# Kernel tuning notes

Hardware: AMD Instinct MI355X
Metric: run time of the kernel (lower is better)

Reference implementation:

```python
import jax, jax.numpy as jnp
import numpy as np

B, S, D, H = 2, 2048, 1024, 16
HD = D // H  # head_dim = 64

def setup_inputs() -> dict:
    key = jax.random.key(0)
    ks = jax.random.split(key, 10)
    s = 1.0 / np.sqrt(D)
    return {
        "hidden_states": jax.random.normal(ks[0], (B, S, D), jnp.float32),
        "attention_mask": jnp.ones((B, S), jnp.float32),
        "q_w": jax.random.uniform(ks[1], (D, D), jnp.float32, -s, s),
        "q_b": jax.random.uniform(ks[2], (D,), jnp.float32, -s, s),
        "k_w": jax.random.uniform(ks[3], (D, D), jnp.float32, -s, s),
        "k_b": jax.random.uniform(ks[4], (D,), jnp.float32, -s, s),
        "v_w": jax.random.uniform(ks[5], (D, D), jnp.float32, -s, s),
        "v_b": jax.random.uniform(ks[6], (D,), jnp.float32, -s, s),
        "o_w": jax.random.uniform(ks[7], (D, D), jnp.float32, -s, s),
        "o_b": jax.random.uniform(ks[8], (D,), jnp.float32, -s, s),
    }

def reference(hidden_states, attention_mask, q_w, q_b, k_w, k_b, v_w, v_b, o_w, o_b):
    scale = HD ** -0.5
    # projections; torch Linear: x @ W^T + b. Here weights stored as (D, D) used directly.
    q = hidden_states @ q_w + q_b  # [B,S,D]
    k = hidden_states @ k_w + k_b
    v = hidden_states @ v_w + v_b
    # split heads -> [B,H,S,HD]
    q = q.reshape(B, S, H, HD).transpose(0, 2, 1, 3)
    k = k.reshape(B, S, H, HD).transpose(0, 2, 1, 3)
    v = v.reshape(B, S, H, HD).transpose(0, 2, 1, 3)
    scores = jnp.einsum('bhqd,bhkd->bhqk', q, k) * scale  # [B,H,S,S]
    # additive mask from 2D [B,S] mask (1=keep, 0=mask)
    scores = scores + (1.0 - attention_mask)[:, None, None, :] * -10000.0
    attn = jax.nn.softmax(scores, axis=-1)
    ctx = jnp.einsum('bhqk,bhkd->bhqd', attn, v)  # [B,H,S,HD]
    ctx = ctx.transpose(0, 2, 1, 3).reshape(B, S, D)
    return ctx @ o_w + o_b
```

## Files before the change

### kernel.cpp

```cpp
#include <hip/hip_runtime.h>
#include <hip/hip_bf16.h>

#define B_ 2
#define S_ 2048
#define D_ 1024
#define H_ 16
#define HD_ 64

#define QSCALE 0.18033688f
#define MLOG2E 14426.950408f

typedef __attribute__((ext_vector_type(8))) short bf16x8;
typedef __attribute__((ext_vector_type(4))) short short4v;
typedef __attribute__((ext_vector_type(4))) float floatx4;

static __device__ __forceinline__ float bf2f(short u) {
  union { float f; unsigned int i; } c;
  c.i = ((unsigned int)(unsigned short)u) << 16;
  return c.f;
}
static __device__ __forceinline__ short f2bf(float f) {
  union { float f; unsigned int i; } c; c.f = f;
  unsigned int r = c.i + 0x7FFFu + ((c.i >> 16) & 1u);
  return (short)(r >> 16);
}
static __device__ __forceinline__ short f2bf_fast(float f) {
  union { float f; unsigned int i; } c; c.f = f;
  return (short)((c.i + 0x8000u) >> 16);
}

static __device__ __forceinline__ void gld_lds16(const void* g, void* l) {
  __builtin_amdgcn_global_load_lds(
      (const __attribute__((address_space(1))) unsigned int*)g,
      (__attribute__((address_space(3))) unsigned int*)l, 16, 0, 0);
}

__global__ __launch_bounds__(256)
void prep(const float* __restrict__ w0, const float* __restrict__ w1,
          const float* __restrict__ w2, const float* __restrict__ w3,
          const float* __restrict__ hs, short* __restrict__ WT,
          short* __restrict__ Xb) {
  const int z = blockIdx.z;
  if (z < 4) {
    __shared__ short t[64][65];
    const float* src = z == 0 ? w0 : z == 1 ? w1 : z == 2 ? w2 : w3;
    short* dst = WT + (size_t)z * D_ * D_;
    const int tx = threadIdx.x & 63, ty = threadIdx.x >> 6;
    const int r0 = blockIdx.y * 64, c0 = blockIdx.x * 64;
    for (int r = ty; r < 64; r += 4)
      t[r][tx] = f2bf(src[(size_t)(r0 + r) * D_ + c0 + tx]);
    __syncthreads();
    for (int r = ty; r < 64; r += 4)
      dst[(size_t)(c0 + r) * D_ + r0 + tx] = t[tx][r];
  } else {
    const int bid = blockIdx.y * 16 + blockIdx.x;
    const float4* in4 = (const float4*)hs;
    short4v* out4 = (short4v*)Xb;
#pragma unroll
    for (int i = 0; i < 16; i++) {
      const int idx = bid * 4096 + i * 256 + threadIdx.x;
      const float4 v = in4[idx];
      short4v o;
      o[0] = f2bf(v.x); o[1] = f2bf(v.y); o[2] = f2bf(v.z); o[3] = f2bf(v.w);
      out4[idx] = o;
    }
  }
}

__global__ __launch_bounds__(256, 3)
void gemm_qkv(const short* __restrict__ X, const short* __restrict__ WT,
              const float* __restrict__ qb, const float* __restrict__ kb,
              const float* __restrict__ vb, const float* __restrict__ mask,
              short* __restrict__ Qo, short* __restrict__ Ko,
              short* __restrict__ Vt) {
  __shared__ __align__(16) short As[128 * 32];
  __shared__ __align__(16) short Bs[128 * 32];
  const int tid = threadIdx.x;
  const int wave = tid >> 6, lane = tid & 63;
  const int col = lane & 15, quad = lane >> 4;
  const int m0 = blockIdx.x * 128;
  const int nt = blockIdx.y;
  const int widx = nt >> 3;
  const int n1 = (nt & 7) * 128;
  const short* Bsrc = WT + (size_t)widx * D_ * D_ + (size_t)n1 * D_;
  const int b = m0 >> 11;

  const int srow = tid >> 2;
  const int skcol = (tid & 3) * 8;
  const short* ga = X + (size_t)(m0 + srow) * D_ + skcol;
  const short* gb = Bsrc + (size_t)srow * D_ + skcol;
  short* la = As + tid * 8;
  short* lb = Bs + tid * 8;

  floatx4 acc[4][4];
#pragma unroll
  for (int i = 0; i < 4; i++)
#pragma unroll
    for (int j = 0; j < 4; j++) acc[i][j] = floatx4{0.f, 0.f, 0.f, 0.f};

  if (widx < 2) {
    const int wseq = (wave >> 1) * 64;
    const int wfeat = (wave & 1) * 64;
    for (int k0 = 0; k0 < D_; k0 += 32) {
      gld_lds16(ga, la);
      gld_lds16(ga + 64 * D_, la + 2048);
      gld_lds16(gb, lb);
      gld_lds16(gb + 64 * D_, lb + 2048);
      ga += 32; gb += 32;
      __syncthreads();
      bf16x8 xf[4], wf[4];
#pragma unroll
      for (int j = 0; j < 4; j++)
        xf[j] = *(const bf16x8*)(As + (wseq + j * 16 + col) * 32 + quad * 8);
#pragma unroll
      for (int i = 0; i < 4; i++)
        wf[i] = *(const bf16x8*)(Bs + (wfeat + i * 16 + col) * 32 + quad * 8);
#pragma unroll
      for (int i = 0; i < 4; i++)
#pragma unroll
        for (int j = 0; j < 4; j++)
          acc[i][j] = __builtin_amdgcn_mfma_f32_16x16x32_bf16(wf[i], xf[j],
                                                              acc[i][j], 0, 0, 0);
      __syncthreads();
    }
    const float* bias = widx == 0 ? qb : kb;
    short* dst = widx == 0 ? Qo : Ko;
    const float scale = widx == 0 ? QSCALE : 1.0f;
#pragma unroll
    for (int i = 0; i < 4; i++) {
      const int nf = n1 + wfeat + i * 16 + quad * 4;
      const int h = nf >> 6, hd = nf & 63;
      const float4 bv = *(const float4*)(bias + nf);
#pragma unroll
      for (int j = 0; j < 4; j++) {
        const int s = (m0 + wseq + j * 16 + col) & (S_ - 1);
        short4v pk;
        pk[0] = f2bf((acc[i][j][0] + bv.x) * scale);
        pk[1] = f2bf((acc[i][j][1] + bv.y) * scale);
        pk[2] = f2bf((acc[i][j][2] + bv.z) * scale);
        pk[3] = f2bf((acc[i][j][3] + bv.w) * scale);
        *(short4v*)(dst + ((size_t)(b * H_ + h) * S_ + s) * HD_ + hd) = pk;
      }
    }
  } else {
    const int wrow = (wave & 1) * 64;
    const int wcol = (wave >> 1) * 64;
    for (int k0 = 0; k0 < D_; k0 += 32) {
      gld_lds16(ga, la);
      gld_lds16(ga + 64 * D_, la + 2048);
      gld_lds16(gb, lb);
      gld_lds16(gb + 64 * D_, lb + 2048);
      ga += 32; gb += 32;
      __syncthreads();
      bf16x8 af[4], bfr[4];
#pragma unroll
      for (int i = 0; i < 4; i++)
        af[i] = *(const bf16x8*)(As + (wrow + i * 16 + col) * 32 + quad * 8);
#pragma unroll
      for (int j = 0; j < 4; j++)
        bfr[j] = *(const bf16x8*)(Bs + (wcol + j * 16 + col) * 32 + quad * 8);
#pragma unroll
      for (int i = 0; i < 4; i++)
#pragma unroll
        for (int j = 0; j < 4; j++)
          acc[i][j] = __builtin_amdgcn_mfma_f32_16x16x32_bf16(af[i], bfr[j],
                                                              acc[i][j], 0, 0, 0);
      __syncthreads();
    }
    float bv[4];
#pragma unroll
    for (int j = 0; j < 4; j++) bv[j] = vb[n1 + wcol + j * 16 + col];
    const float* mkb = mask + (size_t)b * S_;
#pragma unroll
    for (int i = 0; i < 4; i++) {
      const int s = (m0 + wrow + i * 16 + quad * 4) & (S_ - 1);
      const float4 mv = *(const float4*)(mkb + s);
      float w[4];
      w[0] = exp2f((mv.x - 1.0f) * MLOG2E);
      w[1] = exp2f((mv.y - 1.0f) * MLOG2E);
      w[2] = exp2f((mv.z - 1.0f) * MLOG2E);
      w[3] = exp2f((mv.w - 1.0f) * MLOG2E);
#pragma unroll
      for (int j = 0; j < 4; j++) {
        const int nl = n1 + wcol + j * 16 + col;
        const int h = nl >> 6, hd = nl & 63;
        short4v pk;
#pragma unroll
        for (int r = 0; r < 4; r++) pk[r] = f2bf((acc[i][j][r] + bv[j]) * w[r]);
        *(short4v*)(Vt + ((size_t)(b * H_ + h) * HD_ + hd) * S_ + s) = pk;
      }
    }
  }
}

__global__ __launch_bounds__(256, 2)
void attn(const short* __restrict__ Q, const short* __restrict__ K,
          const short* __restrict__ Vt, const float* __restrict__ mask,
          short* __restrict__ ctx) {
  __shared__ __align__(16) short Ks[2][4096];
  __shared__ __align__(16) short Vs[2][4096];
  __shared__ __align__(16) short P[4][2][16][72];
  __shared__ __align__(16) short Ws[S_];
  const int tid = threadIdx.x, wave = tid >> 6, lane = tid & 63;
  const int col = lane & 15, quad = lane >> 4;
  const int lin = blockIdx.x;
  const int qt = (lin >> 3) & 15;
  const int gi = (lin & 7) + ((lin >> 7) << 3);
  const int h = gi & 15, b = gi >> 4;
  const short* Qh = Q + (size_t)(b * H_ + h) * S_ * HD_;
  const short* Kh = K + (size_t)(b * H_ + h) * S_ * HD_;
  const short* Vh = Vt + (size_t)(b * H_ + h) * HD_ * S_;
  const float* mk = mask + (size_t)b * S_;
  const int q0 = qt * 128 + wave * 32;

  const int r1 = tid >> 3, c1 = (tid & 7) ^ (r1 & 7);
  const int r2 = r1 + 32,  c2 = (tid & 7) ^ (r2 & 7);
  const int swz = quad ^ (col & 7);

  gld_lds16(Kh + (size_t)r1 * HD_ + c1 * 8, &Ks[0][tid * 8]);
  gld_lds16(Kh + (size_t)r2 * HD_ + c2 * 8, &Ks[0][(tid + 256) * 8]);
  gld_lds16(Vh + (size_t)r1 * S_ + c1 * 8, &Vs[0][tid * 8]);
  gld_lds16(Vh + (size_t)r2 * S_ + c2 * 8, &Vs[0][(tid + 256) * 8]);

  for (int i = tid; i < S_; i += 256)
    Ws[i] = f2bf(exp2f((mk[i] - 1.0f) * MLOG2E));

  bf16x8 qf[2][2];
#pragma unroll
  for (int g = 0; g < 2; g++) {
    const short* qp = Qh + (size_t)(q0 + g * 16 + col) * HD_;
    qf[g][0] = *(const bf16x8*)(qp + quad * 8);
    qf[g][1] = *(const bf16x8*)(qp + 32 + quad * 8);
  }

  floatx4 acc[2][4], rsacc[2];
#pragma unroll
  for (int g = 0; g < 2; g++) {
    rsacc[g] = floatx4{0.f, 0.f, 0.f, 0.f};
#pragma unroll
    for (int d = 0; d < 4; d++) acc[g][d] = floatx4{0.f, 0.f, 0.f, 0.f};
  }

  __syncthreads();

  for (int it = 0; it < S_ / 64; it++) {
    const int buf = it & 1;
    const int kt = it * 64;
    if (it + 1 < S_ / 64) {
      const int kn = kt + 64;
      gld_lds16(Kh + (size_t)(kn + r1) * HD_ + c1 * 8, &Ks[buf ^ 1][tid * 8]);
      gld_lds16(Kh + (size_t)(kn + r2) * HD_ + c2 * 8, &Ks[buf ^ 1][(tid + 256) * 8]);
      gld_lds16(Vh + (size_t)r1 * S_ + kn + c1 * 8, &Vs[buf ^ 1][tid * 8]);
      gld_lds16(Vh + (size_t)r2 * S_ + kn + c2 * 8, &Vs[buf ^ 1][(tid + 256) * 8]);
    }

    bf16x8 kf[4][2];
#pragma unroll
    for (int t = 0; t < 4; t++) {
      const short* kp = &Ks[buf][(t * 16 + col) * 64];
      kf[t][0] = *(const bf16x8*)(kp + swz * 8);
      kf[t][1] = *(const bf16x8*)(kp + (swz ^ 4) * 8);
    }

#pragma unroll
    for (int g = 0; g < 2; g++)
#pragma unroll
      for (int t = 0; t < 4; t++) {
        floatx4 z = floatx4{0.f, 0.f, 0.f, 0.f};
        z = __builtin_amdgcn_mfma_f32_16x16x32_bf16(kf[t][0], qf[g][0], z, 0, 0, 0);
        z = __builtin_amdgcn_mfma_f32_16x16x32_bf16(kf[t][1], qf[g][1], z, 0, 0, 0);
        short4v pk;
#pragma unroll
        for (int r = 0; r < 4; r++) pk[r] = f2bf_fast(exp2f(z[r]));
        *(short4v*)&P[wave][g][col][t * 16 + quad * 4] = pk;
      }

    bf16x8 pf[2][2];
#pragma unroll
    for (int g = 0; g < 2; g++)
#pragma unroll
      for (int kk = 0; kk < 2; kk++)
        pf[g][kk] = *(const bf16x8*)&P[wave][g][col][kk * 32 + quad * 8];

    bf16x8 wf[2];
#pragma unroll
    for (int kk = 0; kk < 2; kk++)
      wf[kk] = *(const bf16x8*)&Ws[kt + kk * 32 + quad * 8];

#pragma unroll
    for (int g = 0; g < 2; g++) {
      rsacc[g] = __builtin_amdgcn_mfma_f32_16x16x32_bf16(wf[0], pf[g][0], rsacc[g], 0, 0, 0);
      rsacc[g] = __builtin_amdgcn_mfma_f32_16x16x32_bf16(wf[1], pf[g][1], rsacc[g], 0, 0, 0);
    }
#pragma unroll
    for (int d = 0; d < 4; d++) {
      const short* vp = &Vs[buf][(d * 16 + col) * 64];
      const bf16x8 vf0 = *(const bf16x8*)(vp + swz * 8);
      const bf16x8 vf1 = *(const bf16x8*)(vp + (swz ^ 4) * 8);
#pragma unroll
      for (int g = 0; g < 2; g++) {
        acc[g][d] = __builtin_amdgcn_mfma_f32_16x16x32_bf16(vf0, pf[g][0], acc[g][d], 0, 0, 0);
        acc[g][d] = __builtin_amdgcn_mfma_f32_16x16x32_bf16(vf1, pf[g][1], acc[g][d], 0, 0, 0);
      }
    }
    __syncthreads();
  }

#pragma unroll
  for (int g = 0; g < 2; g++) {
    const float inv = 1.0f / (rsacc[g][0] + 1e-30f);
    const size_t row = (size_t)b * S_ + q0 + g * 16 + col;
#pragma unroll
    for (int d = 0; d < 4; d++) {
      short4v o;
#pragma unroll
      for (int r = 0; r < 4; r++) o[r] = f2bf(acc[g][d][r] * inv);
      *(short4v*)(ctx + row * D_ + h * HD_ + d * 16 + quad * 4) = o;
    }
  }
}

__global__ __launch_bounds__(256, 2)
void gemm_out(const short* __restrict__ X, const short* __restrict__ WT,
              const float* __restrict__ ob, float* __restrict__ out) {
  __shared__ __align__(16) short As[64 * 32];
  __shared__ __align__(16) short Bs[128 * 32];
  const int tid = threadIdx.x;
  const int wave = tid >> 6, lane = tid & 63;
  const int col = lane & 15, quad = lane >> 4;
  const int m0 = blockIdx.x * 64;
  const int n0 = blockIdx.y * 128;
  const short* Bsrc = WT + (size_t)n0 * D_;
  const int wrow = (wave & 1) * 32;
  const int wcol = (wave >> 1) * 64;

  floatx4 acc[2][4];
#pragma unroll
  for (int i = 0; i < 2; i++)
#pragma unroll
    for (int j = 0; j < 4; j++) acc[i][j] = floatx4{0.f, 0.f, 0.f, 0.f};

  const int arow = tid >> 2, akcol = (tid & 3) * 8;
  const short* ga = X + (size_t)(m0 + arow) * D_ + akcol;
  const short* gb = Bsrc + (size_t)arow * D_ + akcol;
  short* la = As + tid * 8;
  short* lb = Bs + tid * 8;

  for (int k0 = 0; k0 < D_; k0 += 32) {
    gld_lds16(ga, la);
    gld_lds16(gb, lb);
    gld_lds16(gb + 64 * D_, lb + 2048);
    ga += 32; gb += 32;
    __syncthreads();
    bf16x8 af[2], bfr[4];
#pragma unroll
    for (int i = 0; i < 2; i++)
      af[i] = *(const bf16x8*)(As + (wrow + i * 16 + col) * 32 + quad * 8);
#pragma unroll
    for (int j = 0; j < 4; j++)
      bfr[j] = *(const bf16x8*)(Bs + (wcol + j * 16 + col) * 32 + quad * 8);
#pragma unroll
    for (int i = 0; i < 2; i++)
#pragma unroll
      for (int j = 0; j < 4; j++)
        acc[i][j] = __builtin_amdgcn_mfma_f32_16x16x32_bf16(af[i], bfr[j],
                                                            acc[i][j], 0, 0, 0);
    __syncthreads();
  }

  float bv[4];
#pragma unroll
  for (int j = 0; j < 4; j++) bv[j] = ob[n0 + wcol + j * 16 + col];

#pragma unroll
  for (int i = 0; i < 2; i++) {
    const int m = m0 + wrow + i * 16 + quad * 4;
#pragma unroll
    for (int j = 0; j < 4; j++) {
      const int n = n0 + wcol + j * 16 + col;
#pragma unroll
      for (int r = 0; r < 4; r++)
        out[(size_t)(m + r) * D_ + n] = acc[i][j][r] + bv[j];
    }
  }
}

extern "C" void kernel_launch(void* const* d_in, const int* in_sizes, int n_in,
                              void* d_out, int out_size, void* d_ws, size_t ws_size,
                              hipStream_t stream) {
  (void)in_sizes; (void)n_in; (void)out_size; (void)ws_size;
  const float* hs  = (const float*)d_in[0];
  const float* msk = (const float*)d_in[1];
  const float* qw  = (const float*)d_in[2];
  const float* qb  = (const float*)d_in[3];
  const float* kw  = (const float*)d_in[4];
  const float* kb  = (const float*)d_in[5];
  const float* vw  = (const float*)d_in[6];
  const float* vb  = (const float*)d_in[7];
  const float* ow  = (const float*)d_in[8];
  const float* ob  = (const float*)d_in[9];
  float* out = (float*)d_out;
  char* ws = (char*)d_ws;

  short* Xb  = (short*)(ws);
  short* WT  = (short*)(ws + (8ull  << 20));
  short* Qp  = (short*)(ws + (16ull << 20));
  short* Kp  = (short*)(ws + (24ull << 20));
  short* Vtp = (short*)(ws + (32ull << 20));
  short* Ctx = Xb;

  prep<<<dim3(16, 16, 5), 256, 0, stream>>>(qw, kw, vw, ow, hs, WT, Xb);
  gemm_qkv<<<dim3(32, 24), 256, 0, stream>>>(Xb, WT, qb, kb, vb, msk, Qp, Kp, Vtp);
  attn<<<dim3(512), 256, 0, stream>>>(Qp, Kp, Vtp, msk, Ctx);
  gemm_out<<<dim3(64, 8), 256, 0, stream>>>(Ctx, WT + 3ull * D_ * D_, ob, out);
}
```

Baseline: 212.6 us.

## Double attention query tile per block to 256 rows, halving grid

Each wave now handles 64 query rows instead of 32, so each block covers 256 queries. The grid shrinks from 512 to 256 blocks, which halves redundant K/V tile loads per head and amortizes each LDS K/V fragment over more MFMAs. The P scratch buffer is reused in ping-pong fashion across query groups, with a narrower row pitch and 8-byte reads. The cost is higher register pressure (launch bounds dropped to 1 block/SM) and only 256 blocks, which may underfill the GPU's compute units.

```diff
diff --git a/kernel.cpp b/kernel.cpp
--- a/kernel.cpp
+++ b/kernel.cpp
@@ -193,25 +193,25 @@
   }
 }
 
-__global__ __launch_bounds__(256, 2)
+__global__ __launch_bounds__(256, 1)
 void attn(const short* __restrict__ Q, const short* __restrict__ K,
           const short* __restrict__ Vt, const float* __restrict__ mask,
           short* __restrict__ ctx) {
   __shared__ __align__(16) short Ks[2][4096];
   __shared__ __align__(16) short Vs[2][4096];
-  __shared__ __align__(16) short P[4][2][16][72];
+  __shared__ __align__(16) short P[4][2][16][68];
   __shared__ __align__(16) short Ws[S_];
   const int tid = threadIdx.x, wave = tid >> 6, lane = tid & 63;
   const int col = lane & 15, quad = lane >> 4;
   const int lin = blockIdx.x;
-  const int qt = (lin >> 3) & 15;
-  const int gi = (lin & 7) + ((lin >> 7) << 3);
-  const int h = gi & 15, b = gi >> 4;
-  const short* Qh = Q + (size_t)(b * H_ + h) * S_ * HD_;
-  const short* Kh = K + (size_t)(b * H_ + h) * S_ * HD_;
-  const short* Vh = Vt + (size_t)(b * H_ + h) * HD_ * S_;
+  const int qt = (lin >> 3) & 7;
+  const int bh = (lin & 7) | ((lin >> 6) << 3);
+  const int h = bh & 15, b = bh >> 4;
+  const short* Qh = Q + (size_t)bh * S_ * HD_;
+  const short* Kh = K + (size_t)bh * S_ * HD_;
+  const short* Vh = Vt + (size_t)bh * HD_ * S_;
   const float* mk = mask + (size_t)b * S_;
-  const int q0 = qt * 128 + wave * 32;
+  const int q0 = qt * 256 + wave * 64;
 
   const int r1 = tid >> 3, c1 = (tid & 7) ^ (r1 & 7);
   const int r2 = r1 + 32,  c2 = (tid & 7) ^ (r2 & 7);
@@ -225,17 +225,17 @@
   for (int i = tid; i < S_; i += 256)
     Ws[i] = f2bf(exp2f((mk[i] - 1.0f) * MLOG2E));
 
-  bf16x8 qf[2][2];
-#pragma unroll
-  for (int g = 0; g < 2; g++) {
+  bf16x8 qf[4][2];
+#pragma unroll
+  for (int g = 0; g < 4; g++) {
     const short* qp = Qh + (size_t)(q0 + g * 16 + col) * HD_;
     qf[g][0] = *(const bf16x8*)(qp + quad * 8);
     qf[g][1] = *(const bf16x8*)(qp + 32 + quad * 8);
   }
 
-  floatx4 acc[2][4], rsacc[2];
-#pragma unroll
-  for (int g = 0; g < 2; g++) {
+  floatx4 acc[4][4], rsacc[4];
+#pragma unroll
+  for (int g = 0; g < 4; g++) {
     rsacc[g] = floatx4{0.f, 0.f, 0.f, 0.f};
 #pragma unroll
     for (int d = 0; d < 4; d++) acc[g][d] = floatx4{0.f, 0.f, 0.f, 0.f};
@@ -262,8 +262,12 @@
       kf[t][1] = *(const bf16x8*)(kp + (swz ^ 4) * 8);
     }
 
-#pragma unroll
-    for (int g = 0; g < 2; g++)
+    bf16x8 pf[4][2];
+    bf16x8 wf0 = *(const bf16x8*)&Ws[kt + quad * 8];
+    bf16x8 wf1 = *(const bf16x8*)&Ws[kt + 32 + quad * 8];
+#pragma unroll
+    for (int g = 0; g < 4; g++) {
+      const int pb = g & 1;
 #pragma unroll
       for (int t = 0; t < 4; t++) {
         floatx4 z = floatx4{0.f, 0.f, 0.f, 0.f};
@@ -272,33 +276,28 @@
         short4v pk;
 #pragma unroll
         for (int r = 0; r < 4; r++) pk[r] = f2bf_fast(exp2f(z[r]));
-        *(short4v*)&P[wave][g][col][t * 16 + quad * 4] = pk;
+        *(short4v*)&P[wave][pb][col][t * 16 + quad * 4] = pk;
       }
-
-    bf16x8 pf[2][2];
-#pragma unroll
-    for (int g = 0; g < 2; g++)
-#pragma unroll
-      for (int kk = 0; kk < 2; kk++)
-        pf[g][kk] = *(const bf16x8*)&P[wave][g][col][kk * 32 + quad * 8];
-
-    bf16x8 wf[2];
-#pragma unroll
-    for (int kk = 0; kk < 2; kk++)
-      wf[kk] = *(const bf16x8*)&Ws[kt + kk * 32 + quad * 8];
-
-#pragma unroll
-    for (int g = 0; g < 2; g++) {
-      rsacc[g] = __builtin_amdgcn_mfma_f32_16x16x32_bf16(wf[0], pf[g][0], rsacc[g], 0, 0, 0);
-      rsacc[g] = __builtin_amdgcn_mfma_f32_16x16x32_bf16(wf[1], pf[g][1], rsacc[g], 0, 0, 0);
-    }
+#pragma unroll
+      for (int kk = 0; kk < 2; kk++) {
+        const short4v p0 = *(const short4v*)&P[wave][pb][col][kk * 32 + quad * 8];
+        const short4v p1 = *(const short4v*)&P[wave][pb][col][kk * 32 + quad * 8 + 4];
+        bf16x8 pv;
+        pv[0] = p0[0]; pv[1] = p0[1]; pv[2] = p0[2]; pv[3] = p0[3];
+        pv[4] = p1[0]; pv[5] = p1[1]; pv[6] = p1[2]; pv[7] = p1[3];
+        pf[g][kk] = pv;
+      }
+      rsacc[g] = __builtin_amdgcn_mfma_f32_16x16x32_bf16(wf0, pf[g][0], rsacc[g], 0, 0, 0);
+      rsacc[g] = __builtin_amdgcn_mfma_f32_16x16x32_bf16(wf1, pf[g][1], rsacc[g], 0, 0, 0);
+    }
+
 #pragma unroll
     for (int d = 0; d < 4; d++) {
       const short* vp = &Vs[buf][(d * 16 + col) * 64];
       const bf16x8 vf0 = *(const bf16x8*)(vp + swz * 8);
       const bf16x8 vf1 = *(const bf16x8*)(vp + (swz ^ 4) * 8);
 #pragma unroll
-      for (int g = 0; g < 2; g++) {
+      for (int g = 0; g < 4; g++) {
         acc[g][d] = __builtin_amdgcn_mfma_f32_16x16x32_bf16(vf0, pf[g][0], acc[g][d], 0, 0, 0);
         acc[g][d] = __builtin_amdgcn_mfma_f32_16x16x32_bf16(vf1, pf[g][1], acc[g][d], 0, 0, 0);
       }
@@ -307,7 +306,7 @@
   }
 
 #pragma unroll
-  for (int g = 0; g < 2; g++) {
+  for (int g = 0; g < 4; g++) {
     const float inv = 1.0f / (rsacc[g][0] + 1e-30f);
     const size_t row = (size_t)b * S_ + q0 + g * 16 + col;
 #pragma unroll
@@ -411,6 +410,6 @@
 
   prep<<<dim3(16, 16, 5), 256, 0, stream>>>(qw, kw, vw, ow, hs, WT, Xb);
   gemm_qkv<<<dim3(32, 24), 256, 0, stream>>>(Xb, WT, qb, kb, vb, msk, Qp, Kp, Vtp);
-  attn<<<dim3(512), 256, 0, stream>>>(Qp, Kp, Vtp, msk, Ctx);
+  attn<<<dim3(256), 256, 0, stream>>>(Qp, Kp, Vtp, msk, Ctx);
   gemm_out<<<dim3(64, 8), 256, 0, stream>>>(Ctx, WT + 3ull * D_ * D_, ob, out);
 }
```

Result: slower. 228.8 us (+7.6%).
